# Kernel tuning notes

Measured on AMD Instinct MI355X. Metric: run time of the kernel, lower is better.

## Reference

```python
import jax, jax.numpy as jnp
import numpy as np

N = 100000   # nodes
E = 1600000  # edges
IN, HID, OUT = 128, 128, 64

def setup_inputs() -> dict:
    key = jax.random.key(0)
    ks = jax.random.split(key, 18)
    def lin(k, i, o):
        kw, kb = jax.random.split(k)
        s = 1.0 / np.sqrt(i)
        return (jax.random.uniform(kw, (i, o), jnp.float32, -s, s),
                jax.random.uniform(kb, (o,), jnp.float32, -s, s))
    x = jax.random.normal(ks[0], (N, IN), jnp.float32)
    edge_index = jax.random.randint(ks[1], (2, E), 0, N, jnp.int64)
    W1, b1   = lin(ks[2], IN, HID)
    W21, b21 = lin(ks[3], IN, HID)
    W22, b22 = lin(ks[4], HID, HID)
    W31, b31 = lin(ks[5], IN, HID)
    W32, b32 = lin(ks[6], HID, HID)
    W33, b33 = lin(ks[7], HID, HID)
    Wa, ba   = lin(ks[8], HID, 1)
    Wf, bf   = lin(ks[9], HID, OUT)
    return dict(x=x, edge_index=edge_index, W1=W1, b1=b1, W21=W21, b21=b21,
                W22=W22, b22=b22, W31=W31, b31=b31, W32=W32, b32=b32,
                W33=W33, b33=b33, Wa=Wa, ba=ba, Wf=Wf, bf=bf)

def _gcn(x, W, b, src, dst, dinv):
    # PyG GCNConv: D^{-1/2}(A+I)D^{-1/2} X W + b, self-loops added.
    h = x @ W                                    # [N, F]
    norm = dinv[src] * dinv[dst]                 # [E]
    agg = jax.ops.segment_sum(h[src] * norm[:, None], dst, num_segments=N)
    agg = agg + h * (dinv * dinv)[:, None]       # self-loop contribution
    return agg + b

def reference(x, edge_index, W1, b1, W21, b21, W22, b22, W31, b31,
              W32, b32, W33, b33, Wa, ba, Wf, bf):
    src, dst = edge_index[0], edge_index[1]
    # degree with self-loops (in-degree at target nodes)
    deg = jax.ops.segment_sum(jnp.ones(E, x.dtype), dst, num_segments=N) + 1.0
    dinv = jax.lax.rsqrt(deg)
    h1 = jax.nn.relu(_gcn(x, W1, b1, src, dst, dinv))
    h2 = jax.nn.relu(_gcn(x, W21, b21, src, dst, dinv))
    h2 = jax.nn.relu(_gcn(h2, W22, b22, src, dst, dinv))
    h3 = jax.nn.relu(_gcn(x, W31, b31, src, dst, dinv))
    h3 = jax.nn.relu(_gcn(h3, W32, b32, src, dst, dinv))
    h3 = jax.nn.relu(_gcn(h3, W33, b33, src, dst, dinv))
    H = jnp.stack([h1, h2, h3], axis=1)          # [N, 3, HID]
    scores = H @ Wa + ba                         # [N, 3, 1]
    w = jax.nn.softmax(scores, axis=1)
    h_meta = jnp.sum(w * H, axis=1)              # [N, HID]
    h_out = h_meta + h1
    return h_out @ Wf + bf                       # [N, OUT]
```

## Files before the change

kernel.cpp:

```cpp
#include <hip/hip_runtime.h>
#include <hip/hip_bf16.h>

#define HIDF 128
#define OUTF 64
#define SCAN_B 256

__device__ __forceinline__ float us2f(unsigned u_lo16) {
    return __uint_as_float(u_lo16 << 16);
}
__device__ __forceinline__ unsigned short f2us(float f) {
    __hip_bfloat16 h = __float2bfloat16(f);
    return *reinterpret_cast<unsigned short*>(&h);
}

__global__ __launch_bounds__(256) void deg_zero(int* __restrict__ d, int N) {
    int i = blockIdx.x * 256 + threadIdx.x;
    if (i < N) d[i] = 0;
}

__global__ __launch_bounds__(256) void deg_count(const int* __restrict__ ei, int* __restrict__ d, int E) {
    int e = blockIdx.x * 256 + threadIdx.x;
    if (e < E) atomicAdd(&d[ei[E + e]], 1);
}

__global__ __launch_bounds__(256) void scanA(const int* __restrict__ degi, int* __restrict__ blocksum, int N) {
    __shared__ int red[256];
    const int b = blockIdx.x;
    const int chunk = (N + SCAN_B - 1) / SCAN_B;
    const int lo = b * chunk, hi = min(lo + chunk, N);
    int s = 0;
    for (int i = lo + threadIdx.x; i < hi; i += 256) s += degi[i];
    red[threadIdx.x] = s;
    __syncthreads();
    for (int off = 128; off; off >>= 1) {
        if (threadIdx.x < off) red[threadIdx.x] += red[threadIdx.x + off];
        __syncthreads();
    }
    if (threadIdx.x == 0) blocksum[b] = red[0];
}

__global__ __launch_bounds__(256) void scanB(const int* __restrict__ blocksum, int* __restrict__ blockoff) {
    __shared__ int ps[256];
    const int t = threadIdx.x;
    ps[t] = blocksum[t];
    __syncthreads();
    for (int off = 1; off < 256; off <<= 1) {
        int v = ps[t];
        int u = (t >= off) ? ps[t - off] : 0;
        __syncthreads();
        ps[t] = v + u;
        __syncthreads();
    }
    blockoff[t] = (t == 0) ? 0 : ps[t - 1];
}

__global__ __launch_bounds__(256) void scanC(const int* __restrict__ degi,
                                             const int* __restrict__ blockoff,
                                             int* __restrict__ cursor,
                                             float* __restrict__ dinv, int N) {
    __shared__ int ps[256];
    const int b = blockIdx.x;
    const int chunk = (N + SCAN_B - 1) / SCAN_B;
    const int lo = b * chunk, hi = min(lo + chunk, N);
    const int tchunk = (chunk + 255) / 256;
    const int tlo = lo + threadIdx.x * tchunk;
    const int thi = min(tlo + tchunk, hi);
    int s = 0;
    for (int i = tlo; i < thi; ++i) s += degi[i];
    ps[threadIdx.x] = s;
    __syncthreads();
    for (int off = 1; off < 256; off <<= 1) {
        int v = ps[threadIdx.x];
        int u = (threadIdx.x >= off) ? ps[threadIdx.x - off] : 0;
        __syncthreads();
        ps[threadIdx.x] = v + u;
        __syncthreads();
    }
    int base = blockoff[b] + ((threadIdx.x == 0) ? 0 : ps[threadIdx.x - 1]);
    for (int i = tlo; i < thi; ++i) {
        int d = degi[i];
        cursor[i] = base;
        base += d;
        dinv[i] = rsqrtf((float)d + 1.f);
    }
}

__global__ __launch_bounds__(256) void scatter_kernel(const int* __restrict__ ei,
                                                      int* __restrict__ cursor,
                                                      int* __restrict__ csr_src, int E) {
    int e = blockIdx.x * 256 + threadIdx.x;
    if (e >= E) return;
    int pos = atomicAdd(&cursor[ei[E + e]], 1);
    csr_src[pos] = ei[e];
}

__global__ __launch_bounds__(256) void cvt_scale(const float* __restrict__ X,
                                                 const float* __restrict__ dinv,
                                                 unsigned short* __restrict__ TB, int N) {
    int g = blockIdx.x * 256 + threadIdx.x;
    if (g >= N * 32) return;
    int n = g >> 5;
    float dv = dinv[n];
    float4 v = ((const float4*)X)[g];
    ushort4 o;
    o.x = f2us(v.x * dv); o.y = f2us(v.y * dv);
    o.z = f2us(v.z * dv); o.w = f2us(v.w * dv);
    ((ushort4*)TB)[g] = o;
}

__global__ __launch_bounds__(256) void agg_b(const unsigned short* __restrict__ TB,
                                             const float* __restrict__ dinv,
                                             const int* __restrict__ csr_src,
                                             const int* __restrict__ rend,
                                             float* __restrict__ O, int N) {
    const int n = (blockIdx.x * 256 + threadIdx.x) >> 6;
    const int lane = threadIdx.x & 63;
    if (n >= N) return;
    const int start = (n == 0) ? 0 : rend[n - 1];
    const int end   = rend[n];
    const unsigned* Tv = (const unsigned*)TB;

    float ax0 = 0.f, ay0 = 0.f, ax1 = 0.f, ay1 = 0.f;
    int e = start;
    for (; e + 8 <= end; e += 8) {
        int s0 = csr_src[e + 0], s1 = csr_src[e + 1], s2 = csr_src[e + 2], s3 = csr_src[e + 3];
        int s4 = csr_src[e + 4], s5 = csr_src[e + 5], s6 = csr_src[e + 6], s7 = csr_src[e + 7];
        unsigned v0 = Tv[(size_t)s0 * 64 + lane];
        unsigned v1 = Tv[(size_t)s1 * 64 + lane];
        unsigned v2 = Tv[(size_t)s2 * 64 + lane];
        unsigned v3 = Tv[(size_t)s3 * 64 + lane];
        unsigned v4 = Tv[(size_t)s4 * 64 + lane];
        unsigned v5 = Tv[(size_t)s5 * 64 + lane];
        unsigned v6 = Tv[(size_t)s6 * 64 + lane];
        unsigned v7 = Tv[(size_t)s7 * 64 + lane];
        ax0 += us2f(v0 & 0xffffu); ay0 += __uint_as_float(v0 & 0xffff0000u);
        ax1 += us2f(v1 & 0xffffu); ay1 += __uint_as_float(v1 & 0xffff0000u);
        ax0 += us2f(v2 & 0xffffu); ay0 += __uint_as_float(v2 & 0xffff0000u);
        ax1 += us2f(v3 & 0xffffu); ay1 += __uint_as_float(v3 & 0xffff0000u);
        ax0 += us2f(v4 & 0xffffu); ay0 += __uint_as_float(v4 & 0xffff0000u);
        ax1 += us2f(v5 & 0xffffu); ay1 += __uint_as_float(v5 & 0xffff0000u);
        ax0 += us2f(v6 & 0xffffu); ay0 += __uint_as_float(v6 & 0xffff0000u);
        ax1 += us2f(v7 & 0xffffu); ay1 += __uint_as_float(v7 & 0xffff0000u);
    }
    if (e + 4 <= end) {
        int s0 = csr_src[e + 0], s1 = csr_src[e + 1], s2 = csr_src[e + 2], s3 = csr_src[e + 3];
        unsigned v0 = Tv[(size_t)s0 * 64 + lane];
        unsigned v1 = Tv[(size_t)s1 * 64 + lane];
        unsigned v2 = Tv[(size_t)s2 * 64 + lane];
        unsigned v3 = Tv[(size_t)s3 * 64 + lane];
        ax0 += us2f(v0 & 0xffffu); ay0 += __uint_as_float(v0 & 0xffff0000u);
        ax1 += us2f(v1 & 0xffffu); ay1 += __uint_as_float(v1 & 0xffff0000u);
        ax0 += us2f(v2 & 0xffffu); ay0 += __uint_as_float(v2 & 0xffff0000u);
        ax1 += us2f(v3 & 0xffffu); ay1 += __uint_as_float(v3 & 0xffff0000u);
        e += 4;
    }
    for (; e < end; ++e) {
        int s = csr_src[e];
        unsigned v = Tv[(size_t)s * 64 + lane];
        ax0 += us2f(v & 0xffffu);
        ay0 += __uint_as_float(v & 0xffff0000u);
    }
    unsigned sv = Tv[(size_t)n * 64 + lane];
    ax0 += us2f(sv & 0xffffu);
    ay0 += __uint_as_float(sv & 0xffff0000u);
    const float dv = dinv[n];
    float2 o;
    o.x = (ax0 + ax1) * dv;
    o.y = (ay0 + ay1) * dv;
    ((float2*)O)[(size_t)n * 64 + lane] = o;
}

#define OM_F32 0
#define OM_BF16 1
#define OM_BF16_SR 2
template <int OMODE>
__global__ __launch_bounds__(256) void gemm128d(const float* __restrict__ X,
                                                const float* __restrict__ W,
                                                const float* __restrict__ bias,
                                                const float* __restrict__ dinv,
                                                void* __restrict__ T, int N) {
    __shared__ float Xs[HIDF][68];
    const int tid = threadIdx.x;
    const int nb = blockIdx.x * 64;

    {
        const int nloc = tid & 63;
        const int n = nb + nloc;
        const int kq0 = tid >> 6;
        if (n < N) {
            const float4* Xr = (const float4*)(X + (size_t)n * HIDF);
            #pragma unroll
            for (int kq = kq0; kq < 32; kq += 4) {
                float4 v = Xr[kq];
                int k = kq * 4;
                Xs[k + 0][nloc] = v.x;
                Xs[k + 1][nloc] = v.y;
                Xs[k + 2][nloc] = v.z;
                Xs[k + 3][nloc] = v.w;
            }
        } else {
            #pragma unroll
            for (int kq = kq0; kq < 32; kq += 4) {
                int k = kq * 4;
                Xs[k + 0][nloc] = 0.f; Xs[k + 1][nloc] = 0.f;
                Xs[k + 2][nloc] = 0.f; Xs[k + 3][nloc] = 0.f;
            }
        }
    }
    __syncthreads();

    const int j4  = tid & 31;
    const int sub = tid >> 5;
    const float4* Wrow = (const float4*)W;
    const float4 bv = ((const float4*)bias)[j4];

    float4 acc[8];
    #pragma unroll
    for (int i = 0; i < 8; ++i) acc[i] = bv;

    #pragma unroll 4
    for (int k = 0; k < HIDF; ++k) {
        float4 w = Wrow[k * 32 + j4];
        float xv[8];
        *(float4*)&xv[0] = *(const float4*)&Xs[k][sub * 8];
        *(float4*)&xv[4] = *(const float4*)&Xs[k][sub * 8 + 4];
        #pragma unroll
        for (int i = 0; i < 8; ++i) {
            acc[i].x = fmaf(xv[i], w.x, acc[i].x);
            acc[i].y = fmaf(xv[i], w.y, acc[i].y);
            acc[i].z = fmaf(xv[i], w.z, acc[i].z);
            acc[i].w = fmaf(xv[i], w.w, acc[i].w);
        }
    }

    #pragma unroll
    for (int i = 0; i < 8; ++i) {
        int n = nb + sub * 8 + i;
        if (n >= N) continue;
        float4 o = acc[i];
        if (OMODE == OM_BF16_SR) {
            float dv = dinv[n];
            o.x = fmaxf(o.x, 0.f) * dv; o.y = fmaxf(o.y, 0.f) * dv;
            o.z = fmaxf(o.z, 0.f) * dv; o.w = fmaxf(o.w, 0.f) * dv;
        }
        if (OMODE == OM_F32) {
            *((float4*)((float*)T + (size_t)n * HIDF + j4 * 4)) = o;
        } else {
            ushort4 u;
            u.x = f2us(o.x); u.y = f2us(o.y); u.z = f2us(o.z); u.w = f2us(o.w);
            *((ushort4*)((unsigned short*)T + (size_t)n * HIDF + j4 * 4)) = u;
        }
    }
}

__global__ __launch_bounds__(256) void meta_kernel(const float* __restrict__ H1,
                                                   const unsigned short* __restrict__ H2B,
                                                   const unsigned short* __restrict__ H3B,
                                                   const float* __restrict__ Wa,
                                                   const float* __restrict__ ba,
                                                   const float* __restrict__ Wf,
                                                   const float* __restrict__ bfb,
                                                   float* __restrict__ out, int N) {
    __shared__ float WfS[HIDF * OUTF];
    __shared__ float WaS[HIDF];
    __shared__ float hm[4][HIDF];
    const int tid = threadIdx.x;
    for (int i = tid; i < HIDF * OUTF; i += 256) WfS[i] = Wf[i];
    if (tid < HIDF) WaS[tid] = Wa[tid];
    __syncthreads();
    const float bav = ba[0];
    const int w = tid >> 6;
    const int l = tid & 63;
    const float bfv = bfb[l];
    const int iters = (N + 3) >> 2;

    for (int it = blockIdx.x; it < iters; it += gridDim.x) {
        const int n = it * 4 + w;
        __syncthreads();
        if (n < N) {
            const float* h1 = H1 + (size_t)n * HIDF;
            const unsigned short* h2 = H2B + (size_t)n * HIDF;
            const unsigned short* h3 = H3B + (size_t)n * HIDF;
            float h1a = fmaxf(h1[l], 0.f),            h1b = fmaxf(h1[l + 64], 0.f);
            float h2a = fmaxf(us2f(h2[l]), 0.f),      h2b = fmaxf(us2f(h2[l + 64]), 0.f);
            float h3a = fmaxf(us2f(h3[l]), 0.f),      h3b = fmaxf(us2f(h3[l + 64]), 0.f);
            float s1 = h1a * WaS[l] + h1b * WaS[l + 64];
            float s2 = h2a * WaS[l] + h2b * WaS[l + 64];
            float s3 = h3a * WaS[l] + h3b * WaS[l + 64];
            #pragma unroll
            for (int off = 32; off; off >>= 1) {
                s1 += __shfl_xor(s1, off);
                s2 += __shfl_xor(s2, off);
                s3 += __shfl_xor(s3, off);
            }
            s1 += bav; s2 += bav; s3 += bav;
            float m  = fmaxf(s1, fmaxf(s2, s3));
            float e1 = expf(s1 - m), e2 = expf(s2 - m), e3 = expf(s3 - m);
            float inv = 1.f / (e1 + e2 + e3);
            float w1 = e1 * inv, w2 = e2 * inv, w3 = e3 * inv;
            hm[w][l]      = w1 * h1a + w2 * h2a + w3 * h3a + h1a;
            hm[w][l + 64] = w1 * h1b + w2 * h2b + w3 * h3b + h1b;
        }
        __syncthreads();
        if (n < N) {
            float acc = bfv;
            #pragma unroll
            for (int k = 0; k < HIDF; ++k) acc = fmaf(hm[w][k], WfS[k * OUTF + l], acc);
            out[(size_t)n * OUTF + l] = acc;
        }
    }
}

extern "C" void kernel_launch(void* const* d_in, const int* in_sizes, int n_in,
                              void* d_out, int out_size, void* d_ws, size_t ws_size,
                              hipStream_t stream) {
    const float* x   = (const float*)d_in[0];
    const int*   ei  = (const int*)d_in[1];
    const float *W1  = (const float*)d_in[2],  *b1  = (const float*)d_in[3];
    const float *W21 = (const float*)d_in[4],  *b21 = (const float*)d_in[5];
    const float *W22 = (const float*)d_in[6],  *b22 = (const float*)d_in[7];
    const float *W31 = (const float*)d_in[8],  *b31 = (const float*)d_in[9];
    const float *W32 = (const float*)d_in[10], *b32 = (const float*)d_in[11];
    const float *W33 = (const float*)d_in[12], *b33 = (const float*)d_in[13];
    const float *Wa  = (const float*)d_in[14], *ba  = (const float*)d_in[15];
    const float *Wf  = (const float*)d_in[16], *bfb = (const float*)d_in[17];

    const int N = in_sizes[0] / HIDF;
    const int E = in_sizes[1] / 2;

    int*   DEGI    = (int*)d_ws;
    int*   CURSOR  = DEGI + N;
    int*   CSR_SRC = CURSOR + N;
    int*   BSUM    = CSR_SRC + E;
    int*   BOFF    = BSUM + 256;
    float* DINV    = (float*)(BOFF + 256);
    unsigned short* TB = (unsigned short*)(DINV + N);
    float* PX      = (float*)(TB + (size_t)N * HIDF);
    float* AG      = PX + (size_t)N * HIDF;
    unsigned short* H2B = (unsigned short*)(AG + (size_t)N * HIDF);
    unsigned short* H3B = H2B + (size_t)N * HIDF;

    const int gN    = (N + 255) / 256;
    const int gE    = (E + 255) / 256;
    const int gCVT  = (N * 32 + 255) / 256;
    const int gAGG  = (N * 64 + 255) / 256;
    const int gGEMM = (N + 63) / 64;
    const int gMETA = 2048;

    deg_zero<<<gN, 256, 0, stream>>>(DEGI, N);
    deg_count<<<gE, 256, 0, stream>>>(ei, DEGI, E);
    scanA<<<SCAN_B, 256, 0, stream>>>(DEGI, BSUM, N);
    scanB<<<1, 256, 0, stream>>>(BSUM, BOFF);
    scanC<<<SCAN_B, 256, 0, stream>>>(DEGI, BOFF, CURSOR, DINV, N);
    scatter_kernel<<<gE, 256, 0, stream>>>(ei, CURSOR, CSR_SRC, E);

    cvt_scale<<<gCVT, 256, 0, stream>>>(x, DINV, TB, N);
    agg_b<<<gAGG, 256, 0, stream>>>(TB, DINV, CSR_SRC, CURSOR, PX, N);

    gemm128d<OM_BF16_SR><<<gGEMM, 256, 0, stream>>>(PX, W21, b21, DINV, TB, N);
    agg_b<<<gAGG, 256, 0, stream>>>(TB, DINV, CSR_SRC, CURSOR, AG, N);
    gemm128d<OM_BF16><<<gGEMM, 256, 0, stream>>>(AG, W22, b22, DINV, H2B, N);

    gemm128d<OM_BF16_SR><<<gGEMM, 256, 0, stream>>>(PX, W31, b31, DINV, TB, N);
    agg_b<<<gAGG, 256, 0, stream>>>(TB, DINV, CSR_SRC, CURSOR, AG, N);
    gemm128d<OM_BF16_SR><<<gGEMM, 256, 0, stream>>>(AG, W32, b32, DINV, TB, N);
    agg_b<<<gAGG, 256, 0, stream>>>(TB, DINV, CSR_SRC, CURSOR, AG, N);
    gemm128d<OM_BF16><<<gGEMM, 256, 0, stream>>>(AG, W33, b33, DINV, H3B, N);

    gemm128d<OM_F32><<<gGEMM, 256, 0, stream>>>(PX, W1, b1, DINV, PX, N);

    meta_kernel<<<gMETA, 256, 0, stream>>>(PX, H2B, H3B, Wa, ba, Wf, bfb,
                                           (float*)d_out, N);
}
```

Before: 875.2 us.

## Fuse branch-2/3 first-layer GEMMs and aggregations; store aggregates as bf16

The first-layer GEMMs of branches 2 and 3 (W21 and W31) are merged into one kernel. It writes an interleaved bf16 buffer, which a single dual-feature aggregation then gathers. This replaces two separate GEMM+aggregate passes, so the CSR index list is read once and one gather pass covers both branches. Intermediate aggregates are now stored as bf16 rather than fp32, and the GEMM gains a bf16-input mode, which halves those writes and reads at some cost in precision. The buffer layout is reorganised so it can be reused.

```diff
diff --git a/kernel.cpp b/kernel.cpp
--- a/kernel.cpp
+++ b/kernel.cpp
@@ -11,6 +11,9 @@
 __device__ __forceinline__ unsigned short f2us(float f) {
     __hip_bfloat16 h = __float2bfloat16(f);
     return *reinterpret_cast<unsigned short*>(&h);
+}
+__device__ __forceinline__ unsigned pack2(float a, float b) {
+    return (unsigned)f2us(a) | ((unsigned)f2us(b) << 16);
 }
 
 __global__ __launch_bounds__(256) void deg_zero(int* __restrict__ d, int N) {
@@ -108,11 +111,12 @@
     ((ushort4*)TB)[g] = o;
 }
 
+template <bool OUT_BF16>
 __global__ __launch_bounds__(256) void agg_b(const unsigned short* __restrict__ TB,
                                              const float* __restrict__ dinv,
                                              const int* __restrict__ csr_src,
                                              const int* __restrict__ rend,
-                                             float* __restrict__ O, int N) {
+                                             void* __restrict__ O, int N) {
     const int n = (blockIdx.x * 256 + threadIdx.x) >> 6;
     const int lane = threadIdx.x & 63;
     if (n >= N) return;
@@ -164,21 +168,174 @@
     ax0 += us2f(sv & 0xffffu);
     ay0 += __uint_as_float(sv & 0xffff0000u);
     const float dv = dinv[n];
-    float2 o;
-    o.x = (ax0 + ax1) * dv;
-    o.y = (ay0 + ay1) * dv;
-    ((float2*)O)[(size_t)n * 64 + lane] = o;
-}
-
+    float ox = (ax0 + ax1) * dv;
+    float oy = (ay0 + ay1) * dv;
+    if (OUT_BF16) {
+        ((unsigned*)O)[(size_t)n * 64 + lane] = pack2(ox, oy);
+    } else {
+        float2 o; o.x = ox; o.y = oy;
+        ((float2*)O)[(size_t)n * 64 + lane] = o;
+    }
+}
+
+__global__ __launch_bounds__(256) void agg_dual(const unsigned short* __restrict__ TB23,
+                                                const float* __restrict__ dinv,
+                                                const int* __restrict__ csr_src,
+                                                const int* __restrict__ rend,
+                                                unsigned* __restrict__ OA,
+                                                unsigned* __restrict__ OB, int N) {
+    const int n = (blockIdx.x * 256 + threadIdx.x) >> 6;
+    const int lane = threadIdx.x & 63;
+    if (n >= N) return;
+    const int start = (n == 0) ? 0 : rend[n - 1];
+    const int end   = rend[n];
+    const unsigned* Tv = (const unsigned*)TB23;
+
+    float ax2 = 0.f, ay2 = 0.f, bx2 = 0.f, by2 = 0.f;
+    float ax3 = 0.f, ay3 = 0.f, bx3 = 0.f, by3 = 0.f;
+    int e = start;
+    for (; e + 4 <= end; e += 4) {
+        int s0 = csr_src[e + 0], s1 = csr_src[e + 1], s2 = csr_src[e + 2], s3 = csr_src[e + 3];
+        unsigned a0 = Tv[(size_t)s0 * 128 + lane];
+        unsigned c0 = Tv[(size_t)s0 * 128 + 64 + lane];
+        unsigned a1 = Tv[(size_t)s1 * 128 + lane];
+        unsigned c1 = Tv[(size_t)s1 * 128 + 64 + lane];
+        unsigned a2 = Tv[(size_t)s2 * 128 + lane];
+        unsigned c2 = Tv[(size_t)s2 * 128 + 64 + lane];
+        unsigned a3 = Tv[(size_t)s3 * 128 + lane];
+        unsigned c3 = Tv[(size_t)s3 * 128 + 64 + lane];
+        ax2 += us2f(a0 & 0xffffu); ay2 += __uint_as_float(a0 & 0xffff0000u);
+        ax3 += us2f(c0 & 0xffffu); ay3 += __uint_as_float(c0 & 0xffff0000u);
+        bx2 += us2f(a1 & 0xffffu); by2 += __uint_as_float(a1 & 0xffff0000u);
+        bx3 += us2f(c1 & 0xffffu); by3 += __uint_as_float(c1 & 0xffff0000u);
+        ax2 += us2f(a2 & 0xffffu); ay2 += __uint_as_float(a2 & 0xffff0000u);
+        ax3 += us2f(c2 & 0xffffu); ay3 += __uint_as_float(c2 & 0xffff0000u);
+        bx2 += us2f(a3 & 0xffffu); by2 += __uint_as_float(a3 & 0xffff0000u);
+        bx3 += us2f(c3 & 0xffffu); by3 += __uint_as_float(c3 & 0xffff0000u);
+    }
+    for (; e < end; ++e) {
+        int s = csr_src[e];
+        unsigned a = Tv[(size_t)s * 128 + lane];
+        unsigned c = Tv[(size_t)s * 128 + 64 + lane];
+        ax2 += us2f(a & 0xffffu); ay2 += __uint_as_float(a & 0xffff0000u);
+        ax3 += us2f(c & 0xffffu); ay3 += __uint_as_float(c & 0xffff0000u);
+    }
+    {
+        unsigned a = Tv[(size_t)n * 128 + lane];
+        unsigned c = Tv[(size_t)n * 128 + 64 + lane];
+        ax2 += us2f(a & 0xffffu); ay2 += __uint_as_float(a & 0xffff0000u);
+        ax3 += us2f(c & 0xffffu); ay3 += __uint_as_float(c & 0xffff0000u);
+    }
+    const float dv = dinv[n];
+    OA[(size_t)n * 64 + lane] = pack2((ax2 + bx2) * dv, (ay2 + by2) * dv);
+    OB[(size_t)n * 64 + lane] = pack2((ax3 + bx3) * dv, (ay3 + by3) * dv);
+}
+
+#define IM_F32 0
+#define IM_BF16 1
 #define OM_F32 0
 #define OM_BF16 1
 #define OM_BF16_SR 2
-template <int OMODE>
-__global__ __launch_bounds__(256) void gemm128d(const float* __restrict__ X,
+template <int IMODE, int OMODE>
+__global__ __launch_bounds__(256) void gemm128d(const void* __restrict__ Xv,
                                                 const float* __restrict__ W,
                                                 const float* __restrict__ bias,
                                                 const float* __restrict__ dinv,
                                                 void* __restrict__ T, int N) {
+    __shared__ float Xs[HIDF][68];
+    const int tid = threadIdx.x;
+    const int nb = blockIdx.x * 64;
+
+    {
+        const int nloc = tid & 63;
+        const int n = nb + nloc;
+        const int kq0 = tid >> 6;
+        if (n < N) {
+            if (IMODE == IM_F32) {
+                const float4* Xr = (const float4*)((const float*)Xv + (size_t)n * HIDF);
+                #pragma unroll
+                for (int kq = kq0; kq < 32; kq += 4) {
+                    float4 v = Xr[kq];
+                    int k = kq * 4;
+                    Xs[k + 0][nloc] = v.x;
+                    Xs[k + 1][nloc] = v.y;
+                    Xs[k + 2][nloc] = v.z;
+                    Xs[k + 3][nloc] = v.w;
+                }
+            } else {
+                const ushort4* Xr = (const ushort4*)((const unsigned short*)Xv + (size_t)n * HIDF);
+                #pragma unroll
+                for (int kq = kq0; kq < 32; kq += 4) {
+                    ushort4 v = Xr[kq];
+                    int k = kq * 4;
+                    Xs[k + 0][nloc] = us2f(v.x);
+                    Xs[k + 1][nloc] = us2f(v.y);
+                    Xs[k + 2][nloc] = us2f(v.z);
+                    Xs[k + 3][nloc] = us2f(v.w);
+                }
+            }
+        } else {
+            #pragma unroll
+            for (int kq = kq0; kq < 32; kq += 4) {
+                int k = kq * 4;
+                Xs[k + 0][nloc] = 0.f; Xs[k + 1][nloc] = 0.f;
+                Xs[k + 2][nloc] = 0.f; Xs[k + 3][nloc] = 0.f;
+            }
+        }
+    }
+    __syncthreads();
+
+    const int j4  = tid & 31;
+    const int sub = tid >> 5;
+    const float4* Wrow = (const float4*)W;
+    const float4 bv = ((const float4*)bias)[j4];
+
+    float4 acc[8];
+    #pragma unroll
+    for (int i = 0; i < 8; ++i) acc[i] = bv;
+
+    #pragma unroll 4
+    for (int k = 0; k < HIDF; ++k) {
+        float4 w = Wrow[k * 32 + j4];
+        float xv[8];
+        *(float4*)&xv[0] = *(const float4*)&Xs[k][sub * 8];
+        *(float4*)&xv[4] = *(const float4*)&Xs[k][sub * 8 + 4];
+        #pragma unroll
+        for (int i = 0; i < 8; ++i) {
+            acc[i].x = fmaf(xv[i], w.x, acc[i].x);
+            acc[i].y = fmaf(xv[i], w.y, acc[i].y);
+            acc[i].z = fmaf(xv[i], w.z, acc[i].z);
+            acc[i].w = fmaf(xv[i], w.w, acc[i].w);
+        }
+    }
+
+    #pragma unroll
+    for (int i = 0; i < 8; ++i) {
+        int n = nb + sub * 8 + i;
+        if (n >= N) continue;
+        float4 o = acc[i];
+        if (OMODE == OM_BF16_SR) {
+            float dv = dinv[n];
+            o.x = fmaxf(o.x, 0.f) * dv; o.y = fmaxf(o.y, 0.f) * dv;
+            o.z = fmaxf(o.z, 0.f) * dv; o.w = fmaxf(o.w, 0.f) * dv;
+        }
+        if (OMODE == OM_F32) {
+            *((float4*)((float*)T + (size_t)n * HIDF + j4 * 4)) = o;
+        } else {
+            ushort4 u;
+            u.x = f2us(o.x); u.y = f2us(o.y); u.z = f2us(o.z); u.w = f2us(o.w);
+            *((ushort4*)((unsigned short*)T + (size_t)n * HIDF + j4 * 4)) = u;
+        }
+    }
+}
+
+__global__ __launch_bounds__(256) void gemm_dualA(const float* __restrict__ X,
+                                                  const float* __restrict__ W21,
+                                                  const float* __restrict__ b21,
+                                                  const float* __restrict__ W31,
+                                                  const float* __restrict__ b31,
+                                                  const float* __restrict__ dinv,
+                                                  unsigned short* __restrict__ TB23, int N) {
     __shared__ float Xs[HIDF][68];
     const int tid = threadIdx.x;
     const int nb = blockIdx.x * 64;
@@ -211,25 +368,32 @@
 
     const int j4  = tid & 31;
     const int sub = tid >> 5;
-    const float4* Wrow = (const float4*)W;
-    const float4 bv = ((const float4*)bias)[j4];
-
-    float4 acc[8];
+    const float4* W2r = (const float4*)W21;
+    const float4* W3r = (const float4*)W31;
+    const float4 bv2 = ((const float4*)b21)[j4];
+    const float4 bv3 = ((const float4*)b31)[j4];
+
+    float4 acc2[8], acc3[8];
     #pragma unroll
-    for (int i = 0; i < 8; ++i) acc[i] = bv;
-
-    #pragma unroll 4
+    for (int i = 0; i < 8; ++i) { acc2[i] = bv2; acc3[i] = bv3; }
+
+    #pragma unroll 2
     for (int k = 0; k < HIDF; ++k) {
-        float4 w = Wrow[k * 32 + j4];
+        float4 w2 = W2r[k * 32 + j4];
+        float4 w3 = W3r[k * 32 + j4];
         float xv[8];
         *(float4*)&xv[0] = *(const float4*)&Xs[k][sub * 8];
         *(float4*)&xv[4] = *(const float4*)&Xs[k][sub * 8 + 4];
         #pragma unroll
         for (int i = 0; i < 8; ++i) {
-            acc[i].x = fmaf(xv[i], w.x, acc[i].x);
-            acc[i].y = fmaf(xv[i], w.y, acc[i].y);
-            acc[i].z = fmaf(xv[i], w.z, acc[i].z);
-            acc[i].w = fmaf(xv[i], w.w, acc[i].w);
+            acc2[i].x = fmaf(xv[i], w2.x, acc2[i].x);
+            acc2[i].y = fmaf(xv[i], w2.y, acc2[i].y);
+            acc2[i].z = fmaf(xv[i], w2.z, acc2[i].z);
+            acc2[i].w = fmaf(xv[i], w2.w, acc2[i].w);
+            acc3[i].x = fmaf(xv[i], w3.x, acc3[i].x);
+            acc3[i].y = fmaf(xv[i], w3.y, acc3[i].y);
+            acc3[i].z = fmaf(xv[i], w3.z, acc3[i].z);
+            acc3[i].w = fmaf(xv[i], w3.w, acc3[i].w);
         }
     }
 
@@ -237,19 +401,16 @@
     for (int i = 0; i < 8; ++i) {
         int n = nb + sub * 8 + i;
         if (n >= N) continue;
-        float4 o = acc[i];
-        if (OMODE == OM_BF16_SR) {
-            float dv = dinv[n];
-            o.x = fmaxf(o.x, 0.f) * dv; o.y = fmaxf(o.y, 0.f) * dv;
-            o.z = fmaxf(o.z, 0.f) * dv; o.w = fmaxf(o.w, 0.f) * dv;
-        }
-        if (OMODE == OM_F32) {
-            *((float4*)((float*)T + (size_t)n * HIDF + j4 * 4)) = o;
-        } else {
-            ushort4 u;
-            u.x = f2us(o.x); u.y = f2us(o.y); u.z = f2us(o.z); u.w = f2us(o.w);
-            *((ushort4*)((unsigned short*)T + (size_t)n * HIDF + j4 * 4)) = u;
-        }
+        float dv = dinv[n];
+        float4 o2 = acc2[i], o3 = acc3[i];
+        ushort4 u2, u3;
+        u2.x = f2us(fmaxf(o2.x, 0.f) * dv); u2.y = f2us(fmaxf(o2.y, 0.f) * dv);
+        u2.z = f2us(fmaxf(o2.z, 0.f) * dv); u2.w = f2us(fmaxf(o2.w, 0.f) * dv);
+        u3.x = f2us(fmaxf(o3.x, 0.f) * dv); u3.y = f2us(fmaxf(o3.y, 0.f) * dv);
+        u3.z = f2us(fmaxf(o3.z, 0.f) * dv); u3.w = f2us(fmaxf(o3.w, 0.f) * dv);
+        unsigned short* base = TB23 + (size_t)n * 256;
+        *((ushort4*)(base + j4 * 4)) = u2;
+        *((ushort4*)(base + 128 + j4 * 4)) = u3;
     }
 }
 
@@ -334,11 +495,11 @@
     int*   BSUM    = CSR_SRC + E;
     int*   BOFF    = BSUM + 256;
     float* DINV    = (float*)(BOFF + 256);
-    unsigned short* TB = (unsigned short*)(DINV + N);
-    float* PX      = (float*)(TB + (size_t)N * HIDF);
-    float* AG      = PX + (size_t)N * HIDF;
-    unsigned short* H2B = (unsigned short*)(AG + (size_t)N * HIDF);
-    unsigned short* H3B = H2B + (size_t)N * HIDF;
+    unsigned short* TB23 = (unsigned short*)(DINV + N);
+    float* PX      = (float*)(TB23 + (size_t)N * 256);
+    unsigned* AGA  = (unsigned*)(PX + (size_t)N * HIDF);
+    unsigned* AGB  = AGA + (size_t)N * 64;
+    unsigned* H2B  = AGB + (size_t)N * 64;
 
     const int gN    = (N + 255) / 256;
     const int gE    = (E + 255) / 256;
@@ -354,21 +515,22 @@
     scanC<<<SCAN_B, 256, 0, stream>>>(DEGI, BOFF, CURSOR, DINV, N);
     scatter_kernel<<<gE, 256, 0, stream>>>(ei, CURSOR, CSR_SRC, E);
 
-    cvt_scale<<<gCVT, 256, 0, stream>>>(x, DINV, TB, N);
-    agg_b<<<gAGG, 256, 0, stream>>>(TB, DINV, CSR_SRC, CURSOR, PX, N);
-
-    gemm128d<OM_BF16_SR><<<gGEMM, 256, 0, stream>>>(PX, W21, b21, DINV, TB, N);
-    agg_b<<<gAGG, 256, 0, stream>>>(TB, DINV, CSR_SRC, CURSOR, AG, N);
-    gemm128d<OM_BF16><<<gGEMM, 256, 0, stream>>>(AG, W22, b22, DINV, H2B, N);
-
-    gemm128d<OM_BF16_SR><<<gGEMM, 256, 0, stream>>>(PX, W31, b31, DINV, TB, N);
-    agg_b<<<gAGG, 256, 0, stream>>>(TB, DINV, CSR_SRC, CURSOR, AG, N);
-    gemm128d<OM_BF16_SR><<<gGEMM, 256, 0, stream>>>(AG, W32, b32, DINV, TB, N);
-    agg_b<<<gAGG, 256, 0, stream>>>(TB, DINV, CSR_SRC, CURSOR, AG, N);
-    gemm128d<OM_BF16><<<gGEMM, 256, 0, stream>>>(AG, W33, b33, DINV, H3B, N);
-
-    gemm128d<OM_F32><<<gGEMM, 256, 0, stream>>>(PX, W1, b1, DINV, PX, N);
-
-    meta_kernel<<<gMETA, 256, 0, stream>>>(PX, H2B, H3B, Wa, ba, Wf, bfb,
+    unsigned short* TBX = TB23;
+
+    cvt_scale<<<gCVT, 256, 0, stream>>>(x, DINV, TBX, N);
+    agg_b<false><<<gAGG, 256, 0, stream>>>(TBX, DINV, CSR_SRC, CURSOR, PX, N);
+
+    gemm_dualA<<<gGEMM, 256, 0, stream>>>(PX, W21, b21, W31, b31, DINV, TB23, N);
+    agg_dual<<<gAGG, 256, 0, stream>>>(TB23, DINV, CSR_SRC, CURSOR, AGA, AGB, N);
+
+    gemm128d<IM_BF16, OM_BF16><<<gGEMM, 256, 0, stream>>>(AGA, W22, b22, DINV, H2B, N);
+    gemm128d<IM_BF16, OM_BF16_SR><<<gGEMM, 256, 0, stream>>>(AGB, W32, b32, DINV, TBX, N);
+    agg_b<true><<<gAGG, 256, 0, stream>>>(TBX, DINV, CSR_SRC, CURSOR, AGA, N);
+    gemm128d<IM_BF16, OM_BF16><<<gGEMM, 256, 0, stream>>>(AGA, W33, b33, DINV, AGB, N);
+
+    gemm128d<IM_F32, OM_F32><<<gGEMM, 256, 0, stream>>>(PX, W1, b1, DINV, PX, N);
+
+    meta_kernel<<<gMETA, 256, 0, stream>>>(PX, (const unsigned short*)H2B,
+                                           (const unsigned short*)AGB, Wa, ba, Wf, bfb,
                                            (float*)d_out, N);
 }
```

New measurement: 853.6 us. 1.03x faster.
